# Optimization experiments

Measured on AMD Instinct MI355X. Metric: run time of the kernel, lower is better.

Reference implementation:

```python
import jax, jax.numpy as jnp
import numpy as np

BOX = 256           # box_size
OS = 2              # grid_oversampling_factor
GRID = BOX * OS     # oversampled image size
NPTS = 30000        # n_points
NCLS = 2            # n_classes
NLAT = 16           # n_latent_dims
NLAY = 6            # n_layers
H = 256             # n_neurons_per_layer
L = 10              # pos_enc_dim
BATCH = 4


def positional_encoding(pos, n_freq):
    # NeRF-style: sin/cos(2^k * pi * x) per coordinate -> [N, 6*n_freq]
    freqs = 2.0 ** jnp.arange(n_freq, dtype=pos.dtype)
    ang = pos[..., None] * freqs * jnp.pi                    # [N,3,L]
    enc = jnp.concatenate([jnp.sin(ang), jnp.cos(ang)], axis=-1)
    return enc.reshape(pos.shape[0], 6 * n_freq)


def euler_zyz_to_matrix(ang):
    # ang: [B,3] -> R = Rz(a) @ Ry(b) @ Rz(c), [B,3,3]
    a, b, c = ang[:, 0], ang[:, 1], ang[:, 2]
    ca, sa = jnp.cos(a), jnp.sin(a)
    cb, sb = jnp.cos(b), jnp.sin(b)
    cc, sc = jnp.cos(c), jnp.sin(c)
    row0 = jnp.stack([ca * cb * cc - sa * sc, -ca * cb * sc - sa * cc, ca * sb], -1)
    row1 = jnp.stack([sa * cb * cc + ca * sc, -sa * cb * sc + ca * cc, sa * sb], -1)
    row2 = jnp.stack([-sb * cc, sb * sc, cb], -1)
    return jnp.stack([row0, row1, row2], axis=-2)


def points_to_images(proj, amps):
    # proj: [B,N,2] in [-0.5,0.5]; amps: [B,C,N] -> [B,C,GRID,GRID] via bilinear splat
    B, N, _ = proj.shape
    C = amps.shape[1]
    p = jnp.clip((proj + 0.5) * (GRID - 1), 0.0, GRID - 1.000001)
    x, y = p[..., 0], p[..., 1]
    x0f = jnp.floor(x); y0f = jnp.floor(y)
    fx = x - x0f; fy = y - y0f
    x0 = x0f.astype(jnp.int32); y0 = y0f.astype(jnp.int32)
    x1 = jnp.minimum(x0 + 1, GRID - 1); y1 = jnp.minimum(y0 + 1, GRID - 1)
    w = jnp.stack([(1 - fx) * (1 - fy), fx * (1 - fy), (1 - fx) * fy, fx * fy], -1)  # [B,N,4]
    xi = jnp.stack([x0, x1, x0, x1], -1)
    yi = jnp.stack([y0, y0, y1, y1], -1)
    pix = yi * GRID + xi                                            # [B,N,4]
    bc = (jnp.arange(B)[:, None] * C + jnp.arange(C)[None, :])      # [B,C]
    idx = bc[:, :, None, None] * (GRID * GRID) + pix[:, None, :, :]  # [B,C,N,4]
    vals = amps[:, :, :, None] * w[:, None, :, :]                    # [B,C,N,4]
    img = jnp.zeros((B * C * GRID * GRID,), vals.dtype)
    img = img.at[idx.reshape(-1)].add(vals.reshape(-1))
    return img.reshape(B, C, GRID, GRID)


def fourier_smooth(images, A, B_width):
    # per-class Gaussian low-pass in Fourier, sum classes, crop oversampled grid to BOX
    f = jnp.fft.fftfreq(GRID).astype(images.dtype)
    R = f[None, :] ** 2 + f[:, None] ** 2                            # [G,G]
    filt = A[:, None, None] * jnp.exp(-(B_width[:, None, None] ** 2) * R)
    F = jnp.fft.fft2(images)                                         # [B,C,G,G]
    Fs = jnp.sum(filt * F, axis=1)                                   # [B,G,G]
    Fs = jnp.fft.fftshift(Fs, axes=(-2, -1))
    s = (GRID - BOX) // 2
    Fc = Fs[:, s:s + BOX, s:s + BOX]
    Fc = jnp.fft.ifftshift(Fc, axes=(-2, -1))
    return jnp.real(jnp.fft.ifft2(Fc)) / (OS * OS)


def fourier_shift_2d(im, sx, sy):
    f = jnp.fft.fftfreq(BOX)
    phase = jnp.exp(-2j * jnp.pi * (sx[:, None, None] * f[None, None, :]
                                    + sy[:, None, None] * f[None, :, None]))
    return jnp.real(jnp.fft.ifft2(jnp.fft.fft2(im) * phase))


def setup_inputs() -> dict:
    key = jax.random.key(0)
    ks = jax.random.split(key, 10)
    din = 6 * L + NLAT
    return {
        "z": jax.random.normal(ks[0], (BATCH, NLAT), jnp.float32),
        "orientation": jax.random.uniform(ks[1], (BATCH, 3), jnp.float32, 0.0, 2.0 * np.pi),
        "shift": jax.random.normal(ks[2], (BATCH, 2), jnp.float32) * 2.0,
        "model_positions": jax.random.uniform(ks[3], (NPTS, 3), jnp.float32, -0.4, 0.4),
        "amp": 50.0 * jnp.ones((NCLS, NPTS), jnp.float32),
        "ampvar": jax.random.normal(ks[4], (NCLS, NPTS), jnp.float32),
        "W_in": jax.random.normal(ks[5], (din, H), jnp.float32) / np.sqrt(din),
        "W_layers": jax.random.normal(ks[6], (NLAY, H, H), jnp.float32) / np.sqrt(H),
        "W_out1": jax.random.normal(ks[7], (H, 3), jnp.float32) / np.sqrt(H),
        "W_out2": jax.random.normal(ks[8], (3, 3), jnp.float32) * 0.01,
        "A": jnp.ones((NCLS,), jnp.float32),
        "B_width": 5.0 * jnp.ones((NCLS,), jnp.float32),
    }


def reference(z, orientation, shift, model_positions, amp, ampvar,
              W_in, W_layers, W_out1, W_out2, A, B_width):
    B = z.shape[0]
    # --- displacement MLP (mask=None, warmup=False path) ---
    enc = positional_encoding(model_positions, L)                    # [N,6L]
    feat = jnp.concatenate([
        jnp.broadcast_to(enc[None], (B, NPTS, 6 * L)),
        jnp.broadcast_to(z[:, None, :], (B, NPTS, NLAT)),
    ], axis=-1)                                                      # [B,N,6L+lat]
    h = feat @ W_in                                                  # input Linear (no bias)
    for i in range(NLAY):                                            # LinearBlock = ELU(Linear)
        h = jax.nn.elu(h @ W_layers[i])
    disp = jax.nn.elu(h @ W_out1) @ W_out2                           # [B,N,3]
    final_pos = model_positions[None] + disp                         # [B,N,3]
    # --- projection ---
    Rm = euler_zyz_to_matrix(orientation)                            # [B,3,3]
    proj = jnp.einsum('bnd,bde->bne', final_pos, Rm)[..., :2]        # [B,N,2]
    # --- amplitudes, splat, smooth, shift ---
    wamp = amp * jax.nn.softmax(ampvar, axis=0)                      # [C,N]
    wamp = jnp.broadcast_to(wamp[None], (B, NCLS, NPTS))
    imgs = points_to_images(proj, wamp)                              # [B,C,G,G]
    sm = fourier_smooth(imgs, A, B_width)                            # [B,BOX,BOX]
    out = fourier_shift_2d(sm, shift[:, 0], shift[:, 1])
    return out, final_pos, disp
```

## Files before the change

kernel.cpp:

```cpp
#include <hip/hip_runtime.h>

#define PI_F 3.14159265358979323846f

constexpr int GRIDN = 512;
constexpr int BOXN  = 256;
constexpr int NPTS  = 30000;
constexpr int NCLS  = 2;
constexpr int NLAT  = 16;
constexpr int HDIM  = 256;
constexpr int LFREQ = 10;
constexpr int BATCH = 4;
constexpr int NROWS = BATCH*NPTS;
constexpr int RM    = 48;

#define ASC   2048.0f
#define AINV  (1.0f/2048.0f)
#define OINV  (1.0f/33554432.0f)
#define BSC   16384.0f

typedef _Float16 f16x8 __attribute__((ext_vector_type(8)));
typedef float    f32x4 __attribute__((ext_vector_type(4)));

__device__ __forceinline__ float elu_f(float x){ return x > 0.f ? x : (__expf(x) - 1.0f); }

__device__ __forceinline__ void split_f16(float vs, uint32_t& hb, uint32_t& lb){
    const _Float16 h = (_Float16)vs;
    const _Float16 l = (_Float16)(vs - (float)h);
    union { _Float16 f; uint16_t u; } uh, ul;
    uh.f = h; ul.f = l;
    hb = uh.u; lb = ul.u;
}
__device__ __forceinline__ uint32_t pack_act(float v){
    uint32_t hb, lb;
    split_f16(v * ASC, hb, lb);
    return hb | (lb << 16);
}
__device__ __forceinline__ float unpack_act(uint32_t u){
    union { uint16_t u16; _Float16 f; } a, b;
    a.u16 = (uint16_t)(u & 0xffffu);
    b.u16 = (uint16_t)(u >> 16);
    return ((float)a.f + (float)b.f) * AINV;
}

__host__ __device__ __forceinline__ size_t wp_off(int lay){
    return (lay == 0) ? 0 : (size_t)(98304 + (lay-1)*262144);
}

__global__ void prepack_kernel(const float* __restrict__ Win,
                               const float* __restrict__ Wlay,
                               unsigned char* __restrict__ wp)
{
    const int tid = blockIdx.x*256 + threadIdx.x;
    if (tid >= 7*8*16*64) return;
    const int lane  = tid & 63;
    const int n16   = (tid >> 6) & 15;
    const int kstep = (tid >> 10) & 7;
    const int lay   = tid >> 13;
    if (lay == 0 && kstep >= 3) return;
    const int kbase = 32*kstep + 8*(lane >> 4);
    const int c = 16*n16 + (lane & 15);
    uint32_t hw[4], lw[4];
    #pragma unroll
    for (int p = 0; p < 4; ++p) {
        uint32_t hh0=0, hh1=0, ll0=0, ll1=0;
        #pragma unroll
        for (int q = 0; q < 2; ++q) {
            const int k = kbase + 2*p + q;
            float w = 0.f;
            if (lay == 0) { if (k < 76) w = Win[k*HDIM + c]; }
            else w = Wlay[(size_t)(lay-1)*HDIM*HDIM + (size_t)k*HDIM + c];
            uint32_t hb, lb;
            split_f16(w * BSC, hb, lb);
            if (q == 0) { hh0 = hb; ll0 = lb; } else { hh1 = hb; ll1 = lb; }
        }
        hw[p] = hh0 | (hh1 << 16);
        lw[p] = ll0 | (ll1 << 16);
    }
    uint4* dst = (uint4*)(wp + wp_off(lay)) + (size_t)((kstep*16 + n16)*2)*64 + lane;
    dst[0]  = make_uint4(hw[0], hw[1], hw[2], hw[3]);
    dst[64] = make_uint4(lw[0], lw[1], lw[2], lw[3]);
}

__launch_bounds__(512, 4)
__global__ void mlp_fused(const float* __restrict__ pos,
                          const float* __restrict__ zlat,
                          const unsigned char* __restrict__ wp,
                          const float* __restrict__ Wout1,
                          const float* __restrict__ Wout2,
                          const float* __restrict__ orient,
                          float* __restrict__ out_fp,
                          float* __restrict__ out_disp,
                          float2* __restrict__ proj)
{
    __shared__ uint4 h4[RM*64];
    __shared__ float w1s[HDIM*3];
    uint32_t* hs = (uint32_t*)h4;
    const int t = threadIdx.x;
    const int lane = t & 63;
    const int wv = t >> 6;
    const int row0 = blockIdx.x * RM;
    const int g  = lane >> 4;
    const int rb = lane & 15;

    for (int idx = t; idx < RM*96; idx += 512) {
        const int r = idx / 96, c = idx - r*96;
        const int row = row0 + r;
        const int b = row / NPTS, n = row - b*NPTS;
        float v = 0.f;
        if (c < 60) {
            const int d = c / 20, rem = c - d*20;
            const int f = (rem < 10) ? rem : rem - 10;
            const float ang = pos[n*3+d] * (float)(1<<f) * PI_F;
            v = (rem < 10) ? sinf(ang) : cosf(ang);
        } else if (c < 76) {
            v = zlat[b*NLAT + (c - 60)];
        }
        hs[r*256 + (c ^ ((r&7)<<2))] = pack_act(v);
    }
    for (int idx = t; idx < HDIM*3; idx += 512) w1s[idx] = Wout1[idx];
    __syncthreads();

    for (int lay = 0; lay < 7; ++lay) {
        const int KS = lay ? 8 : 3;
        const uint4* bp = (const uint4*)(wp + wp_off(lay));

        f32x4 acc[6];
        #pragma unroll
        for (int i = 0; i < 6; ++i) { f32x4 zz = {0.f,0.f,0.f,0.f}; acc[i] = zz; }

        uint4 BH0[2], BL0[2], BH1[2], BL1[2];

        auto LOADB = [&](uint4 (&H)[2], uint4 (&L)[2], int k){
            #pragma unroll
            for (int f = 0; f < 2; ++f) {
                const size_t s0 = (size_t)((k*16 + 2*wv + f)*2)*64 + lane;
                H[f] = bp[s0];
                L[f] = bp[s0 + 64];
            }
        };
        auto STEP = [&](const uint4 (&H)[2], const uint4 (&L)[2], int k){
            #pragma unroll
            for (int m = 0; m < 3; ++m) {
                const int r = 16*m + rb;
                const int s = r & 7;
                const int G0 = 8*k + 2*g;
                const uint4 p0 = h4[r*64 + (G0 ^ s)];
                const uint4 p1 = h4[r*64 + ((G0+1) ^ s)];
                const uint32_t e0=p0.x, e1=p0.y, e2=p0.z, e3=p0.w;
                const uint32_t e4=p1.x, e5=p1.y, e6=p1.z, e7=p1.w;
                union { uint4 q; f16x8 v; } ah, al;
                ah.q = make_uint4((e0 & 0xffffu) | (e1 << 16),
                                  (e2 & 0xffffu) | (e3 << 16),
                                  (e4 & 0xffffu) | (e5 << 16),
                                  (e6 & 0xffffu) | (e7 << 16));
                al.q = make_uint4((e0 >> 16) | (e1 & 0xffff0000u),
                                  (e2 >> 16) | (e3 & 0xffff0000u),
                                  (e4 >> 16) | (e5 & 0xffff0000u),
                                  (e6 >> 16) | (e7 & 0xffff0000u));
                #pragma unroll
                for (int nn = 0; nn < 2; ++nn) {
                    union { uint4 q; f16x8 v; } bh, bl;
                    bh.q = H[nn]; bl.q = L[nn];
                    f32x4 a = acc[m*2+nn];
                    a = __builtin_amdgcn_mfma_f32_16x16x32_f16(ah.v, bl.v, a, 0, 0, 0);
                    a = __builtin_amdgcn_mfma_f32_16x16x32_f16(al.v, bh.v, a, 0, 0, 0);
                    a = __builtin_amdgcn_mfma_f32_16x16x32_f16(ah.v, bh.v, a, 0, 0, 0);
                    acc[m*2+nn] = a;
                }
            }
        };

        LOADB(BH0, BL0, 0);
        for (int k = 0; k < KS; k += 2) {
            if (k+1 < KS) LOADB(BH1, BL1, k+1);
            STEP(BH0, BL0, k);
            if (k+1 < KS) {
                if (k+2 < KS) LOADB(BH0, BL0, k+2);
                STEP(BH1, BL1, k+1);
            }
        }

        __syncthreads();
        const bool do_elu = (lay >= 1);
        #pragma unroll
        for (int m = 0; m < 3; ++m) {
            #pragma unroll
            for (int nn = 0; nn < 2; ++nn) {
                #pragma unroll
                for (int j = 0; j < 4; ++j) {
                    float v = acc[m*2+nn][j] * OINV;
                    if (do_elu) v = elu_f(v);
                    const int r = 16*m + 4*g + j;
                    const int c = 32*wv + 16*nn + rb;
                    hs[r*256 + (c ^ ((r&7)<<2))] = pack_act(v);
                }
            }
        }
        __syncthreads();
    }

    if (t < RM) {
        const int row = row0 + t;
        const int b = row / NPTS, n = row - b*NPTS;
        const int s = (t & 7) << 2;
        float o0=0.f, o1=0.f, o2=0.f;
        for (int k = 0; k < HDIM; ++k) {
            const float hv = unpack_act(hs[t*256 + (k ^ s)]);
            o0 = fmaf(hv, w1s[k*3+0], o0);
            o1 = fmaf(hv, w1s[k*3+1], o1);
            o2 = fmaf(hv, w1s[k*3+2], o2);
        }
        o0 = elu_f(o0); o1 = elu_f(o1); o2 = elu_f(o2);
        const float d0 = o0*Wout2[0] + o1*Wout2[3] + o2*Wout2[6];
        const float d1 = o0*Wout2[1] + o1*Wout2[4] + o2*Wout2[7];
        const float d2 = o0*Wout2[2] + o1*Wout2[5] + o2*Wout2[8];
        const float p0 = pos[n*3+0] + d0;
        const float p1 = pos[n*3+1] + d1;
        const float p2 = pos[n*3+2] + d2;
        out_disp[(size_t)row*3+0] = d0; out_disp[(size_t)row*3+1] = d1; out_disp[(size_t)row*3+2] = d2;
        out_fp[(size_t)row*3+0]   = p0; out_fp[(size_t)row*3+1]   = p1; out_fp[(size_t)row*3+2]   = p2;
        float sa,ca,sb,cb,sc,cc;
        sincosf(orient[b*3+0], &sa, &ca);
        sincosf(orient[b*3+1], &sb, &cb);
        sincosf(orient[b*3+2], &sc, &cc);
        const float R00 =  ca*cb*cc - sa*sc;
        const float R10 =  sa*cb*cc + ca*sc;
        const float R20 = -sb*cc;
        const float R01 = -ca*cb*sc - sa*cc;
        const float R11 = -sa*cb*sc + ca*cc;
        const float R21 =  sb*sc;
        float2 pr;
        pr.x = p0*R00 + p1*R10 + p2*R20;
        pr.y = p0*R01 + p1*R11 + p2*R21;
        proj[row] = pr;
    }
}

__global__ void scatter_kernel(const float2* __restrict__ proj,
                               const float* __restrict__ amp,
                               const float* __restrict__ ampvar,
                               float* __restrict__ img)
{
    const int i = blockIdx.x * 256 + threadIdx.x;
    if (i >= NROWS) return;
    const int b = i / NPTS;
    const int n = i - b*NPTS;
    const float2 pr = proj[i];
    float x = (pr.x + 0.5f) * (float)(GRIDN-1);
    float y = (pr.y + 0.5f) * (float)(GRIDN-1);
    x = fminf(fmaxf(x, 0.f), 511.0f);
    y = fminf(fmaxf(y, 0.f), 511.0f);
    const float x0f = floorf(x), y0f = floorf(y);
    const float fx = x - x0f, fy = y - y0f;
    const int x0 = (int)x0f, y0 = (int)y0f;
    const int x1 = min(x0+1, GRIDN-1), y1 = min(y0+1, GRIDN-1);
    const float av0 = ampvar[n], av1 = ampvar[NPTS + n];
    const float m  = fmaxf(av0, av1);
    const float e0 = __expf(av0 - m), e1 = __expf(av1 - m);
    const float inv = 1.0f / (e0 + e1);
    const float w0 = amp[n]        * e0 * inv;
    const float w1 = amp[NPTS + n] * e1 * inv;
    const float w00 = (1.f-fx)*(1.f-fy), w10 = fx*(1.f-fy), w01 = (1.f-fx)*fy, w11 = fx*fy;
    float* img0 = img + (size_t)(b*NCLS + 0)*GRIDN*GRIDN;
    float* img1 = img + (size_t)(b*NCLS + 1)*GRIDN*GRIDN;
    const int i00 = y0*GRIDN + x0, i10 = y0*GRIDN + x1;
    const int i01 = y1*GRIDN + x0, i11 = y1*GRIDN + x1;
    atomicAdd(img0 + i00, w0*w00); atomicAdd(img0 + i10, w0*w10);
    atomicAdd(img0 + i01, w0*w01); atomicAdd(img0 + i11, w0*w11);
    atomicAdd(img1 + i00, w1*w00); atomicAdd(img1 + i10, w1*w10);
    atomicAdd(img1 + i01, w1*w01); atomicAdd(img1 + i11, w1*w11);
}

template<int N, bool INV, bool RIN, bool ROUT>
__global__ void fft_pass(const float* __restrict__ in, float* __restrict__ out,
                         int in_per, long in_s1, long in_s2, long in_es,
                         int out_per, long out_s1, long out_s2, long out_es,
                         float scale)
{
    __shared__ float2 s[N];
    const int t  = threadIdx.x;
    const int rb = blockIdx.x;
    const long ib = (long)(rb / in_per) * in_s1 + (long)(rb % in_per) * in_s2;
    constexpr int LOG2N = (N == 512) ? 9 : 8;
    #pragma unroll
    for (int j = 0; j < 2; ++j) {
        const int i  = t + j*(N/2);
        const int ri = (int)(__brev((unsigned)i) >> (32 - LOG2N));
        float2 v;
        if (RIN) { v.x = in[ib + (long)i*in_es]; v.y = 0.f; }
        else       v = ((const float2*)in)[ib + (long)i*in_es];
        s[ri] = v;
    }
    for (int len = 1; len < N; len <<= 1) {
        __syncthreads();
        const int p  = t & (len-1);
        const int i0 = ((t & ~(len-1)) << 1) | p;
        const float ang = (INV ? PI_F : -PI_F) * (float)p / (float)len;
        float sn, cs; __sincosf(ang, &sn, &cs);
        const float2 a  = s[i0];
        const float2 bv = s[i0 + len];
        const float2 bt = make_float2(bv.x*cs - bv.y*sn, bv.x*sn + bv.y*cs);
        s[i0]       = make_float2(a.x + bt.x, a.y + bt.y);
        s[i0 + len] = make_float2(a.x - bt.x, a.y - bt.y);
    }
    __syncthreads();
    const long ob = (long)(rb / out_per) * out_s1 + (long)(rb % out_per) * out_s2;
    #pragma unroll
    for (int j = 0; j < 2; ++j) {
        const int i = t + j*(N/2);
        if (ROUT) out[ob + (long)i*out_es] = s[i].x * scale;
        else {
            float2 v = s[i]; v.x *= scale; v.y *= scale;
            ((float2*)out)[ob + (long)i*out_es] = v;
        }
    }
}

__global__ void combine_kernel(const float2* __restrict__ F,
                               const float* __restrict__ Afac,
                               const float* __restrict__ Bw,
                               const float* __restrict__ shift,
                               float2* __restrict__ Q)
{
    const int u = blockIdx.x;
    const int b = blockIdx.y;
    const int v = threadIdx.x;
    const int mu  = (u < 128) ? u : u + 256;
    const int mv  = (v < 128) ? v : v + 256;
    const int u2  = (256 - u) & 255;
    const int v2  = (256 - v) & 255;
    const int mu2 = (u2 < 128) ? u2 : u2 + 256;
    const int mv2 = (v2 < 128) ? v2 : v2 + 256;
    const float fy1 = (float)((mu  < 256) ? mu  : mu  - 512) / 512.0f;
    const float fx1 = (float)((mv  < 256) ? mv  : mv  - 512) / 512.0f;
    const float fy2 = (float)((mu2 < 256) ? mu2 : mu2 - 512) / 512.0f;
    const float fx2 = (float)((mv2 < 256) ? mv2 : mv2 - 512) / 512.0f;
    const float R1 = fy1*fy1 + fx1*fx1;
    const float R2 = fy2*fy2 + fx2*fx2;
    float a1x=0.f, a1y=0.f, a2x=0.f, a2y=0.f;
    #pragma unroll
    for (int c = 0; c < NCLS; ++c) {
        const float bw = Bw[c];
        const float f1 = Afac[c] * __expf(-bw*bw*R1);
        const float f2 = Afac[c] * __expf(-bw*bw*R2);
        const float2* Fi = F + ((size_t)(b*NCLS + c) << 18);
        const float2 v1 = Fi[mu *512 + mv ];
        const float2 vh = Fi[mu2*512 + mv2];
        a1x = fmaf(f1, v1.x, a1x); a1y = fmaf(f1, v1.y, a1y);
        a2x = fmaf(f2, vh.x, a2x); a2y = fmaf(f2, vh.y, a2y);
    }
    const float Gx = 0.5f*(a1x + a2x);
    const float Gy = 0.5f*(a1y - a2y);
    const float fu = (float)((u < 128) ? u : u - 256) / 256.0f;
    const float fv = (float)((v < 128) ? v : v - 256) / 256.0f;
    const float th = -2.0f*PI_F*(shift[b*2+0]*fv + shift[b*2+1]*fu);
    float sn, cs; __sincosf(th, &sn, &cs);
    float2 o;
    o.x = Gx*cs - Gy*sn;
    o.y = Gx*sn + Gy*cs;
    Q[((size_t)b << 16) + (size_t)u*256 + v] = o;
}

extern "C" void kernel_launch(void* const* d_in, const int* in_sizes, int n_in,
                              void* d_out, int out_size, void* d_ws, size_t ws_size,
                              hipStream_t stream)
{
    (void)in_sizes; (void)n_in; (void)out_size; (void)ws_size;
    const float* z      = (const float*)d_in[0];
    const float* orient = (const float*)d_in[1];
    const float* shift  = (const float*)d_in[2];
    const float* pos    = (const float*)d_in[3];
    const float* amp    = (const float*)d_in[4];
    const float* ampvar = (const float*)d_in[5];
    const float* Win    = (const float*)d_in[6];
    const float* Wlay   = (const float*)d_in[7];
    const float* Wout1  = (const float*)d_in[8];
    const float* Wout2  = (const float*)d_in[9];
    const float* Afac   = (const float*)d_in[10];
    const float* Bw     = (const float*)d_in[11];

    float* out      = (float*)d_out;
    float* out_img  = out;
    float* out_fp   = out + (size_t)BATCH*BOXN*BOXN;
    float* out_disp = out_fp + (size_t)NROWS*3;

    char*   ws   = (char*)d_ws;
    float*  img  = (float*)ws;
    float2* bufA = (float2*)(ws + (size_t)8*1024*1024);
    unsigned char* wp = (unsigned char*)(ws + (size_t)8*1024*1024);
    float2* Q    = (float2*)(ws + (size_t)25165824);
    float2* proj = (float2*)(ws + (size_t)27262976);

    (void)hipMemsetAsync(img, 0, (size_t)BATCH*NCLS*GRIDN*GRIDN*sizeof(float), stream);

    prepack_kernel<<<(7*8*16*64 + 255)/256, 256, 0, stream>>>(Win, Wlay, wp);

    mlp_fused<<<NROWS/RM, 512, 0, stream>>>(pos, z, wp, Wout1, Wout2, orient,
                                            out_fp, out_disp, proj);
    scatter_kernel<<<(NROWS+255)/256, 256, 0, stream>>>(proj, amp, ampvar, img);

    fft_pass<512,false,true ,false><<<BATCH*NCLS*512, 256, 0, stream>>>(
        img, (float*)bufA, 512, 262144, 512, 1, 512, 262144, 512, 1, 1.0f);
    fft_pass<512,false,false,false><<<BATCH*NCLS*512, 256, 0, stream>>>(
        (const float*)bufA, (float*)bufA, 512, 262144, 1, 512, 512, 262144, 1, 512, 1.0f);

    combine_kernel<<<dim3(256, BATCH), 256, 0, stream>>>(bufA, Afac, Bw, shift, Q);

    fft_pass<256,true ,false,false><<<BATCH*256, 128, 0, stream>>>(
        (const float*)Q, (float*)Q, 256, 65536, 256, 1, 256, 65536, 256, 1, 1.0f/256.0f);
    fft_pass<256,true ,false,true ><<<BATCH*256, 128, 0, stream>>>(
        (const float*)Q, out_img, 256, 65536, 1, 256, 256, 65536, 1, 256, 0.25f/256.0f);
}
```

Measured before the change: 516.4 us.

## Fold split-f16 activation hi/lo into MFMA K dimension to cut MFMA count

Restructures the split-fp16 emulated-fp32 GEMM so that each activation's packed (hi,lo) f16 pair is fed directly as two K elements of the MFMA A operand. The weights are prepacked with each hi or lo value duplicated into both halves of a pair. This removes the per-step unpacking shuffles of A and reduces the inner loop from three MFMAs per tile to two. The trade-off is that each MFMA now covers half as many real K values, so total MFMA instructions, weight loads and weight-buffer size change, and the layer-0 padding layout changes.

```diff
diff --git a/kernel.cpp b/kernel.cpp
--- a/kernel.cpp
+++ b/kernel.cpp
@@ -43,7 +43,7 @@
 }
 
 __host__ __device__ __forceinline__ size_t wp_off(int lay){
-    return (lay == 0) ? 0 : (size_t)(98304 + (lay-1)*262144);
+    return (lay == 0) ? 0 : (size_t)(6*16*2048 + (size_t)(lay-1)*16*16*2048);
 }
 
 __global__ void prepack_kernel(const float* __restrict__ Win,
@@ -51,34 +51,30 @@
                                unsigned char* __restrict__ wp)
 {
     const int tid = blockIdx.x*256 + threadIdx.x;
-    if (tid >= 7*8*16*64) return;
-    const int lane  = tid & 63;
-    const int n16   = (tid >> 6) & 15;
-    const int kstep = (tid >> 10) & 7;
-    const int lay   = tid >> 13;
-    if (lay == 0 && kstep >= 3) return;
-    const int kbase = 32*kstep + 8*(lane >> 4);
+    if (tid >= 102*16*64) return;
+    const int lane = tid & 63;
+    const int n16  = (tid >> 6) & 15;
+    const int widx = tid >> 10;
+    int lay, wi;
+    if (widx < 6) { lay = 0; wi = widx; }
+    else          { lay = 1 + (widx-6)/16; wi = (widx-6) & 15; }
+    const int g = lane >> 4;
     const int c = 16*n16 + (lane & 15);
-    uint32_t hw[4], lw[4];
+    uint32_t b1[4], b3[4];
     #pragma unroll
     for (int p = 0; p < 4; ++p) {
-        uint32_t hh0=0, hh1=0, ll0=0, ll1=0;
-        #pragma unroll
-        for (int q = 0; q < 2; ++q) {
-            const int k = kbase + 2*p + q;
-            float w = 0.f;
-            if (lay == 0) { if (k < 76) w = Win[k*HDIM + c]; }
-            else w = Wlay[(size_t)(lay-1)*HDIM*HDIM + (size_t)k*HDIM + c];
-            uint32_t hb, lb;
-            split_f16(w * BSC, hb, lb);
-            if (q == 0) { hh0 = hb; ll0 = lb; } else { hh1 = hb; ll1 = lb; }
-        }
-        hw[p] = hh0 | (hh1 << 16);
-        lw[p] = ll0 | (ll1 << 16);
-    }
-    uint4* dst = (uint4*)(wp + wp_off(lay)) + (size_t)((kstep*16 + n16)*2)*64 + lane;
-    dst[0]  = make_uint4(hw[0], hw[1], hw[2], hw[3]);
-    dst[64] = make_uint4(lw[0], lw[1], lw[2], lw[3]);
+        const int kap = 16*wi + 4*g + p;
+        float w = 0.f;
+        if (lay == 0) { if (kap < 76) w = Win[kap*HDIM + c]; }
+        else w = Wlay[(size_t)(lay-1)*HDIM*HDIM + (size_t)kap*HDIM + c];
+        uint32_t hb, lb;
+        split_f16(w * BSC, hb, lb);
+        b1[p] = hb | (hb << 16);
+        b3[p] = lb | (lb << 16);
+    }
+    uint4* dst = (uint4*)(wp + wp_off(lay)) + (size_t)(wi*16 + n16)*128 + lane;
+    dst[0]  = make_uint4(b1[0], b1[1], b1[2], b1[3]);
+    dst[64] = make_uint4(b3[0], b3[1], b3[2], b3[3]);
 }
 
 __launch_bounds__(512, 4)
@@ -128,55 +124,49 @@
         #pragma unroll
         for (int i = 0; i < 6; ++i) { f32x4 zz = {0.f,0.f,0.f,0.f}; acc[i] = zz; }
 
-        uint4 BH0[2], BL0[2], BH1[2], BL1[2];
-
-        auto LOADB = [&](uint4 (&H)[2], uint4 (&L)[2], int k){
+        uint4 B1A[2][2], B3A[2][2], B1B[2][2], B3B[2][2];
+
+        auto LOADB = [&](uint4 (&B1)[2][2], uint4 (&B3)[2][2], int k){
             #pragma unroll
-            for (int f = 0; f < 2; ++f) {
-                const size_t s0 = (size_t)((k*16 + 2*wv + f)*2)*64 + lane;
-                H[f] = bp[s0];
-                L[f] = bp[s0 + 64];
+            for (int w = 0; w < 2; ++w) {
+                const int wi = 2*k + w;
+                #pragma unroll
+                for (int nn = 0; nn < 2; ++nn) {
+                    const size_t s0 = (size_t)(wi*16 + 2*wv + nn)*128 + lane;
+                    B1[w][nn] = bp[s0];
+                    B3[w][nn] = bp[s0 + 64];
+                }
             }
         };
-        auto STEP = [&](const uint4 (&H)[2], const uint4 (&L)[2], int k){
+        auto STEP = [&](const uint4 (&B1)[2][2], const uint4 (&B3)[2][2], int k){
             #pragma unroll
             for (int m = 0; m < 3; ++m) {
                 const int r = 16*m + rb;
                 const int s = r & 7;
-                const int G0 = 8*k + 2*g;
-                const uint4 p0 = h4[r*64 + (G0 ^ s)];
-                const uint4 p1 = h4[r*64 + ((G0+1) ^ s)];
-                const uint32_t e0=p0.x, e1=p0.y, e2=p0.z, e3=p0.w;
-                const uint32_t e4=p1.x, e5=p1.y, e6=p1.z, e7=p1.w;
-                union { uint4 q; f16x8 v; } ah, al;
-                ah.q = make_uint4((e0 & 0xffffu) | (e1 << 16),
-                                  (e2 & 0xffffu) | (e3 << 16),
-                                  (e4 & 0xffffu) | (e5 << 16),
-                                  (e6 & 0xffffu) | (e7 << 16));
-                al.q = make_uint4((e0 >> 16) | (e1 & 0xffff0000u),
-                                  (e2 >> 16) | (e3 & 0xffff0000u),
-                                  (e4 >> 16) | (e5 & 0xffff0000u),
-                                  (e6 >> 16) | (e7 & 0xffff0000u));
                 #pragma unroll
-                for (int nn = 0; nn < 2; ++nn) {
-                    union { uint4 q; f16x8 v; } bh, bl;
-                    bh.q = H[nn]; bl.q = L[nn];
-                    f32x4 a = acc[m*2+nn];
-                    a = __builtin_amdgcn_mfma_f32_16x16x32_f16(ah.v, bl.v, a, 0, 0, 0);
-                    a = __builtin_amdgcn_mfma_f32_16x16x32_f16(al.v, bh.v, a, 0, 0, 0);
-                    a = __builtin_amdgcn_mfma_f32_16x16x32_f16(ah.v, bh.v, a, 0, 0, 0);
-                    acc[m*2+nn] = a;
+                for (int w = 0; w < 2; ++w) {
+                    union { uint4 q; f16x8 v; } A;
+                    A.q = h4[r*64 + ((8*k + 4*w + g) ^ s)];
+                    #pragma unroll
+                    for (int nn = 0; nn < 2; ++nn) {
+                        union { uint4 q; f16x8 v; } c1, c3;
+                        c1.q = B1[w][nn]; c3.q = B3[w][nn];
+                        f32x4 a = acc[m*2+nn];
+                        a = __builtin_amdgcn_mfma_f32_16x16x32_f16(A.v, c1.v, a, 0, 0, 0);
+                        a = __builtin_amdgcn_mfma_f32_16x16x32_f16(A.v, c3.v, a, 0, 0, 0);
+                        acc[m*2+nn] = a;
+                    }
                 }
             }
         };
 
-        LOADB(BH0, BL0, 0);
+        LOADB(B1A, B3A, 0);
         for (int k = 0; k < KS; k += 2) {
-            if (k+1 < KS) LOADB(BH1, BL1, k+1);
-            STEP(BH0, BL0, k);
+            if (k+1 < KS) LOADB(B1B, B3B, k+1);
+            STEP(B1A, B3A, k);
             if (k+1 < KS) {
-                if (k+2 < KS) LOADB(BH0, BL0, k+2);
-                STEP(BH1, BL1, k+1);
+                if (k+2 < KS) LOADB(B1A, B3A, k+2);
+                STEP(B1B, B3B, k+1);
             }
         }
 
@@ -393,7 +383,7 @@
 
     (void)hipMemsetAsync(img, 0, (size_t)BATCH*NCLS*GRIDN*GRIDN*sizeof(float), stream);
 
-    prepack_kernel<<<(7*8*16*64 + 255)/256, 256, 0, stream>>>(Win, Wlay, wp);
+    prepack_kernel<<<(102*16*64 + 255)/256, 256, 0, stream>>>(Win, Wlay, wp);
 
     mlp_fused<<<NROWS/RM, 512, 0, stream>>>(pos, z, wp, Wout1, Wout2, orient,
                                             out_fp, out_disp, proj);
```

After: 594.7 us. 15.2% more time.

## Pack two real class images into one complex FFT and separate spectra via symmetry

Applied to the files above, without the earlier changes.

The two real class images per batch are packed as real and imaginary parts of one complex image, so the 2D forward FFT runs on half as many transforms. The combine kernel then recovers each class spectrum from Z[k] and conj(Z[-k]) using Hermitian symmetry, at the cost of two extra gathers per output point. This halves forward FFT row and column work and the intermediate buffer traffic.

```diff
diff --git a/kernel.cpp b/kernel.cpp
--- a/kernel.cpp
+++ b/kernel.cpp
@@ -271,6 +271,41 @@
     atomicAdd(img1 + i01, w1*w01); atomicAdd(img1 + i11, w1*w11);
 }
 
+__global__ void fft_row_pair(const float* __restrict__ img, float2* __restrict__ Z)
+{
+    __shared__ float2 s[512];
+    const int t  = threadIdx.x;
+    const int rb = blockIdx.x;
+    const int b  = rb >> 9, y = rb & 511;
+    const float* p0 = img + ((size_t)(b*2+0) << 18) + (size_t)y*512;
+    const float* p1 = img + ((size_t)(b*2+1) << 18) + (size_t)y*512;
+    #pragma unroll
+    for (int j = 0; j < 2; ++j) {
+        const int i  = t + j*256;
+        const int ri = (int)(__brev((unsigned)i) >> 23);
+        s[ri] = make_float2(p0[i], p1[i]);
+    }
+    for (int len = 1; len < 512; len <<= 1) {
+        __syncthreads();
+        const int p  = t & (len-1);
+        const int i0 = ((t & ~(len-1)) << 1) | p;
+        const float ang = -PI_F * (float)p / (float)len;
+        float sn, cs; __sincosf(ang, &sn, &cs);
+        const float2 a  = s[i0];
+        const float2 bv = s[i0 + len];
+        const float2 bt = make_float2(bv.x*cs - bv.y*sn, bv.x*sn + bv.y*cs);
+        s[i0]       = make_float2(a.x + bt.x, a.y + bt.y);
+        s[i0 + len] = make_float2(a.x - bt.x, a.y - bt.y);
+    }
+    __syncthreads();
+    float2* zo = Z + ((size_t)b << 18) + (size_t)y*512;
+    #pragma unroll
+    for (int j = 0; j < 2; ++j) {
+        const int i = t + j*256;
+        zo[i] = s[i];
+    }
+}
+
 template<int N, bool INV, bool RIN, bool ROUT>
 __global__ void fft_pass(const float* __restrict__ in, float* __restrict__ out,
                          int in_per, long in_s1, long in_s2, long in_es,
@@ -316,7 +351,7 @@
     }
 }
 
-__global__ void combine_kernel(const float2* __restrict__ F,
+__global__ void combine_kernel(const float2* __restrict__ Z,
                                const float* __restrict__ Afac,
                                const float* __restrict__ Bw,
                                const float* __restrict__ shift,
@@ -331,6 +366,23 @@
     const int v2  = (256 - v) & 255;
     const int mu2 = (u2 < 128) ? u2 : u2 + 256;
     const int mv2 = (v2 < 128) ? v2 : v2 + 256;
+    const int nmu  = (512 - mu)  & 511;
+    const int nmv  = (512 - mv)  & 511;
+    const int nmu2 = (512 - mu2) & 511;
+    const int nmv2 = (512 - mv2) & 511;
+
+    const float2* Zb = Z + ((size_t)b << 18);
+    const float2 A   = Zb[(size_t)mu  *512 + mv ];
+    const float2 Am  = Zb[(size_t)nmu *512 + nmv];
+    const float2 A2  = Zb[(size_t)mu2 *512 + mv2];
+    const float2 A2m = Zb[(size_t)nmu2*512 + nmv2];
+
+    float2 F1v[2], FHv[2];
+    F1v[0] = make_float2(0.5f*(A.x + Am.x),  0.5f*(A.y - Am.y));
+    F1v[1] = make_float2(0.5f*(A.y + Am.y), -0.5f*(A.x - Am.x));
+    FHv[0] = make_float2(0.5f*(A2.x + A2m.x),  0.5f*(A2.y - A2m.y));
+    FHv[1] = make_float2(0.5f*(A2.y + A2m.y), -0.5f*(A2.x - A2m.x));
+
     const float fy1 = (float)((mu  < 256) ? mu  : mu  - 512) / 512.0f;
     const float fx1 = (float)((mv  < 256) ? mv  : mv  - 512) / 512.0f;
     const float fy2 = (float)((mu2 < 256) ? mu2 : mu2 - 512) / 512.0f;
@@ -343,11 +395,8 @@
         const float bw = Bw[c];
         const float f1 = Afac[c] * __expf(-bw*bw*R1);
         const float f2 = Afac[c] * __expf(-bw*bw*R2);
-        const float2* Fi = F + ((size_t)(b*NCLS + c) << 18);
-        const float2 v1 = Fi[mu *512 + mv ];
-        const float2 vh = Fi[mu2*512 + mv2];
-        a1x = fmaf(f1, v1.x, a1x); a1y = fmaf(f1, v1.y, a1y);
-        a2x = fmaf(f2, vh.x, a2x); a2y = fmaf(f2, vh.y, a2y);
+        a1x = fmaf(f1, F1v[c].x, a1x); a1y = fmaf(f1, F1v[c].y, a1y);
+        a2x = fmaf(f2, FHv[c].x, a2x); a2y = fmaf(f2, FHv[c].y, a2y);
     }
     const float Gx = 0.5f*(a1x + a2x);
     const float Gy = 0.5f*(a1y - a2y);
@@ -386,7 +435,7 @@
 
     char*   ws   = (char*)d_ws;
     float*  img  = (float*)ws;
-    float2* bufA = (float2*)(ws + (size_t)8*1024*1024);
+    float2* Zb   = (float2*)(ws + (size_t)8*1024*1024);
     unsigned char* wp = (unsigned char*)(ws + (size_t)8*1024*1024);
     float2* Q    = (float2*)(ws + (size_t)25165824);
     float2* proj = (float2*)(ws + (size_t)27262976);
@@ -399,12 +448,11 @@
                                             out_fp, out_disp, proj);
     scatter_kernel<<<(NROWS+255)/256, 256, 0, stream>>>(proj, amp, ampvar, img);
 
-    fft_pass<512,false,true ,false><<<BATCH*NCLS*512, 256, 0, stream>>>(
-        img, (float*)bufA, 512, 262144, 512, 1, 512, 262144, 512, 1, 1.0f);
-    fft_pass<512,false,false,false><<<BATCH*NCLS*512, 256, 0, stream>>>(
-        (const float*)bufA, (float*)bufA, 512, 262144, 1, 512, 512, 262144, 1, 512, 1.0f);
-
-    combine_kernel<<<dim3(256, BATCH), 256, 0, stream>>>(bufA, Afac, Bw, shift, Q);
+    fft_row_pair<<<BATCH*512, 256, 0, stream>>>(img, Zb);
+    fft_pass<512,false,false,false><<<BATCH*512, 256, 0, stream>>>(
+        (const float*)Zb, (float*)Zb, 512, 262144, 1, 512, 512, 262144, 1, 512, 1.0f);
+
+    combine_kernel<<<dim3(256, BATCH), 256, 0, stream>>>(Zb, Afac, Bw, shift, Q);
 
     fft_pass<256,true ,false,false><<<BATCH*256, 128, 0, stream>>>(
         (const float*)Q, (float*)Q, 256, 65536, 256, 1, 256, 65536, 256, 1, 1.0f/256.0f);
```

Result: faster. 482.7 us (-6.5%).
